# Performance work log

Measured on AMD Instinct MI355X. Metric: run time of the kernel, lower is better.

## Reference

```python
import jax, jax.numpy as jnp
import numpy as np

B, S, H = 32, 2048, 1024

def setup_inputs() -> dict:
    key = jax.random.key(0)
    ks = jax.random.split(key, 8)
    scale = 1.0 / np.sqrt(H)
    return {
        "decoder_hidden": jax.random.normal(ks[0], (B, 1, H), dtype=jnp.float32),
        "encoder_outputs": jax.random.normal(ks[1], (B, S, H), dtype=jnp.float32),
        "coverage": jax.random.uniform(ks[2], (B, S), dtype=jnp.float32),
        "W_enc": jax.random.normal(ks[3], (H, H), dtype=jnp.float32) * scale,  # enc_v.weight [out,in]
        "W_dec": jax.random.normal(ks[4], (H, H), dtype=jnp.float32) * scale,  # dec_v.weight
        "b_dec": jax.random.normal(ks[5], (H,), dtype=jnp.float32) * scale,    # dec_v.bias
        "w_cov": jax.random.normal(ks[6], (H,), dtype=jnp.float32) * scale,    # cov_v.weight [H,1] squeezed
        "v": jax.random.normal(ks[7], (H,), dtype=jnp.float32) * scale,        # V_prime.weight [1,H] squeezed
    }

def reference(decoder_hidden, encoder_outputs, coverage, W_enc, W_dec, b_dec, w_cov, v):
    # enc_feature: [B,S,H]; torch Linear is x @ W.T
    enc_feature = jnp.einsum("bsh,oh->bso", encoder_outputs, W_enc)
    # dec_feature: [B,1,H], broadcasts over S
    dec_feature = jnp.einsum("bqh,oh->bqo", decoder_hidden, W_dec) + b_dec
    # cov_feature: coverage[...,None] @ w_cov[None,:] -> [B,S,H]
    cov_feature = coverage[..., None] * w_cov
    scores = jnp.tanh(enc_feature + dec_feature + cov_feature)  # [B,S,H]
    attn_scores = jnp.einsum("bsh,h->bs", scores, v)            # V_prime, squeeze(-1)
    attn_dist = jax.nn.softmax(attn_scores, axis=-1)[:, None, :]  # [B,1,S]
    return attn_dist
```

## Files before the change

kernel.cpp:

```cpp
#include <hip/hip_runtime.h>

#define Bb 32
#define Ss 2048
#define Hh 1024

typedef __attribute__((ext_vector_type(4))) float f32x4;
typedef __attribute__((ext_vector_type(8))) short s16x8;

#define GAS const __attribute__((address_space(1))) unsigned int
#define LAS __attribute__((address_space(3))) unsigned int

__device__ __forceinline__ unsigned short f2bf(float x) {
  unsigned int u = __float_as_uint(x);
  u = (u + 0x7fffu + ((u >> 16) & 1u)) >> 16;
  return (unsigned short)u;
}

__global__ void cvt_swz_kernel(const float* __restrict__ in, unsigned short* __restrict__ out) {
  int g = blockIdx.x * blockDim.x + threadIdx.x;
  int row = g >> 7;
  int kc8 = (g & 127) << 3;
  const float4* src = reinterpret_cast<const float4*>(in + (size_t)row * Hh + kc8);
  float4 a = src[0], b = src[1];
  union { unsigned short u[8]; uint4 q; } rr;
  rr.u[0] = f2bf(a.x); rr.u[1] = f2bf(a.y); rr.u[2] = f2bf(a.z); rr.u[3] = f2bf(a.w);
  rr.u[4] = f2bf(b.x); rr.u[5] = f2bf(b.y); rr.u[6] = f2bf(b.z); rr.u[7] = f2bf(b.w);
  int r = row & 255;
  size_t byte = ((size_t)(row >> 8) * 32 + (kc8 >> 5)) * 16384
              + (size_t)(r * 64 + (((kc8 & 31) * 2) ^ ((r & 3) << 4)));
  *reinterpret_cast<uint4*>(reinterpret_cast<char*>(out) + byte) = rr.q;
}

__global__ void dec_feat_kernel(const float* __restrict__ dh,
                                const float* __restrict__ Wd,
                                const float* __restrict__ bd,
                                float* __restrict__ out) {
  int gw = blockIdx.x * 4 + (threadIdx.x >> 6);
  int lane = threadIdx.x & 63;
  int b = gw >> 10;
  int o = gw & 1023;
  const float4* x = reinterpret_cast<const float4*>(dh + (size_t)b * Hh);
  const float4* w = reinterpret_cast<const float4*>(Wd + (size_t)o * Hh);
  float acc = 0.f;
#pragma unroll
  for (int it = 0; it < 4; ++it) {
    float4 xa = x[lane + it * 64];
    float4 wa = w[lane + it * 64];
    acc += xa.x * wa.x + xa.y * wa.y + xa.z * wa.z + xa.w * wa.w;
  }
#pragma unroll
  for (int m = 1; m < 64; m <<= 1) acc += __shfl_xor(acc, m, 64);
  if (lane == 0) out[gw] = acc + bd[o];
}

__global__ void __launch_bounds__(512, 2)
gemm8(const unsigned short* __restrict__ Aw,
      const unsigned short* __restrict__ Bw,
      const float* __restrict__ decf,
      const float* __restrict__ cov,
      const float* __restrict__ wcov,
      const float* __restrict__ v,
      float* __restrict__ scores) {
  __shared__ char lds[131072];

  const int bid = blockIdx.x;
  const int swz = (bid & 7) * 128 + (bid >> 3);
  const int s_tile = swz >> 2;
  const int ot = swz & 3;

  const int tid = threadIdx.x, lane = tid & 63;
  const int wid = tid >> 6, wm = wid >> 2, wn = wid & 3;
  const int fr = lane & 15, hi = lane >> 4;

  const char* gA = reinterpret_cast<const char*>(Aw) + (size_t)s_tile * 32 * 16384 + tid * 16;
  const char* gB = reinterpret_cast<const char*>(Bw) + (size_t)ot * 32 * 16384 + tid * 16;

#define STAGE_A(t) do {                                                           \
    const char* _s = gA + (size_t)(t) * 16384;                                    \
    char* _d = lds + ((t) & 3) * 32768 + tid * 16;                                \
    __builtin_amdgcn_global_load_lds((GAS*)(_s),        (LAS*)(_d),        16, 0, 0); \
    __builtin_amdgcn_global_load_lds((GAS*)(_s + 8192), (LAS*)(_d + 8192), 16, 0, 0); \
  } while (0)
#define STAGE_B(t) do {                                                           \
    const char* _s = gB + (size_t)(t) * 16384;                                    \
    char* _d = lds + ((t) & 3) * 32768 + 16384 + tid * 16;                        \
    __builtin_amdgcn_global_load_lds((GAS*)(_s),        (LAS*)(_d),        16, 0, 0); \
    __builtin_amdgcn_global_load_lds((GAS*)(_s + 8192), (LAS*)(_d + 8192), 16, 0, 0); \
  } while (0)
#define NOSTAGE ((void)0)
#define VM4 asm volatile("s_waitcnt vmcnt(4)" ::: "memory")
#define VM0 asm volatile("s_waitcnt vmcnt(0)" ::: "memory")
#define NOWAIT ((void)0)

  const int xr = (fr & 3) << 4;
  const int aOff = wm * 8192 + fr * 64 + ((hi * 16) ^ xr);
  const int bOff = 16384 + wn * 4096 + fr * 64 + ((hi * 16) ^ xr);

  f32x4 acc[8][4];
#pragma unroll
  for (int i = 0; i < 8; ++i)
#pragma unroll
    for (int j = 0; j < 4; ++j) acc[i][j] = (f32x4){0.f, 0.f, 0.f, 0.f};

  s16x8 afrag[4], bfrag[4];

#define PH_A(t, STAGE) do {                                                       \
    const char* Lb = lds + ((t) & 3) * 32768;                                     \
    _Pragma("unroll") for (int fn = 0; fn < 4; ++fn)                              \
      bfrag[fn] = *reinterpret_cast<const s16x8*>(Lb + bOff + fn * 1024);         \
    _Pragma("unroll") for (int fm = 0; fm < 4; ++fm)                              \
      afrag[fm] = *reinterpret_cast<const s16x8*>(Lb + aOff + fm * 1024);         \
    STAGE;                                                                        \
    __builtin_amdgcn_s_barrier();                                                 \
    asm volatile("s_waitcnt lgkmcnt(0)" ::: "memory");                            \
    __builtin_amdgcn_sched_barrier(0);                                            \
    __builtin_amdgcn_s_setprio(1);                                                \
    _Pragma("unroll") for (int fm = 0; fm < 4; ++fm)                              \
      _Pragma("unroll") for (int fn = 0; fn < 4; ++fn)                            \
        acc[fm][fn] = __builtin_amdgcn_mfma_f32_16x16x32_bf16(                    \
            afrag[fm], bfrag[fn], acc[fm][fn], 0, 0, 0);                          \
    __builtin_amdgcn_s_setprio(0);                                                \
    __builtin_amdgcn_s_barrier();                                                 \
  } while (0)

#define PH_B(t, STAGE, WAIT) do {                                                 \
    const char* Lb = lds + ((t) & 3) * 32768;                                     \
    _Pragma("unroll") for (int fm = 0; fm < 4; ++fm)                              \
      afrag[fm] = *reinterpret_cast<const s16x8*>(Lb + aOff + (fm + 4) * 1024);   \
    STAGE;                                                                        \
    WAIT;                                                                         \
    __builtin_amdgcn_s_barrier();                                                 \
    asm volatile("s_waitcnt lgkmcnt(0)" ::: "memory");                            \
    __builtin_amdgcn_sched_barrier(0);                                            \
    __builtin_amdgcn_s_setprio(1);                                                \
    _Pragma("unroll") for (int fm = 0; fm < 4; ++fm)                              \
      _Pragma("unroll") for (int fn = 0; fn < 4; ++fn)                            \
        acc[fm + 4][fn] = __builtin_amdgcn_mfma_f32_16x16x32_bf16(                \
            afrag[fm], bfrag[fn], acc[fm + 4][fn], 0, 0, 0);                      \
    __builtin_amdgcn_s_setprio(0);                                                \
    __builtin_amdgcn_s_barrier();                                                 \
  } while (0)

  STAGE_A(0); STAGE_B(0);
  STAGE_A(1); STAGE_B(1);
  VM4;
  __builtin_amdgcn_s_barrier();

  for (int t = 0; t < 30; ++t) {
    PH_A(t, STAGE_A(t + 2));
    PH_B(t, STAGE_B(t + 2), VM4);
  }
  PH_A(30, NOSTAGE);
  PH_B(30, NOSTAGE, VM0);
  PH_A(31, NOSTAGE);
  PH_B(31, NOSTAGE, NOWAIT);

#undef PH_A
#undef PH_B
#undef STAGE_A
#undef STAGE_B

  const int row0 = s_tile * 256 + wm * 128 + hi * 4;
  const int o0 = ot * 256 + wn * 64 + fr;
  const int bb = s_tile >> 3;

  float vv[4], wv[4], dv[4];
#pragma unroll
  for (int fn = 0; fn < 4; ++fn) {
    int o = o0 + fn * 16;
    vv[fn] = v[o];
    wv[fn] = wcov[o];
    dv[fn] = decf[bb * 1024 + o];
  }

#pragma unroll
  for (int fm = 0; fm < 8; ++fm) {
#pragma unroll
    for (int r = 0; r < 4; ++r) {
      int s_flat = row0 + fm * 16 + r;
      float c = cov[s_flat];
      float sum = 0.f;
#pragma unroll
      for (int fn = 0; fn < 4; ++fn) {
        float x = acc[fm][fn][r] + dv[fn] + c * wv[fn];
        sum += tanhf(x) * vv[fn];
      }
      sum += __shfl_xor(sum, 1, 64);
      sum += __shfl_xor(sum, 2, 64);
      sum += __shfl_xor(sum, 4, 64);
      sum += __shfl_xor(sum, 8, 64);
      if (fr == 0) atomicAdd(&scores[s_flat], sum);
    }
  }
}

__global__ void softmax_kernel(const float* __restrict__ scores, float* __restrict__ out) {
  int b = blockIdx.x;
  int tid = threadIdx.x;
  int lane = tid & 63, w = tid >> 6;
  const float* row = scores + (size_t)b * Ss;
  float vals[8];
#pragma unroll
  for (int k = 0; k < 8; ++k) vals[k] = row[tid + k * 256];
  float m = vals[0];
#pragma unroll
  for (int k = 1; k < 8; ++k) m = fmaxf(m, vals[k]);
#pragma unroll
  for (int off = 1; off < 64; off <<= 1) m = fmaxf(m, __shfl_xor(m, off, 64));
  __shared__ float sm[4], ss[4];
  if (lane == 0) sm[w] = m;
  __syncthreads();
  m = fmaxf(fmaxf(sm[0], sm[1]), fmaxf(sm[2], sm[3]));
  float s = 0.f;
#pragma unroll
  for (int k = 0; k < 8; ++k) { vals[k] = __expf(vals[k] - m); s += vals[k]; }
#pragma unroll
  for (int off = 1; off < 64; off <<= 1) s += __shfl_xor(s, off, 64);
  if (lane == 0) ss[w] = s;
  __syncthreads();
  s = ss[0] + ss[1] + ss[2] + ss[3];
  float inv = 1.f / s;
#pragma unroll
  for (int k = 0; k < 8; ++k) out[(size_t)b * Ss + tid + k * 256] = vals[k] * inv;
}

extern "C" void kernel_launch(void* const* d_in, const int* in_sizes, int n_in,
                              void* d_out, int out_size, void* d_ws, size_t ws_size,
                              hipStream_t stream) {
  const float* dh    = (const float*)d_in[0];
  const float* enc   = (const float*)d_in[1];
  const float* cov   = (const float*)d_in[2];
  const float* W_enc = (const float*)d_in[3];
  const float* W_dec = (const float*)d_in[4];
  const float* b_dec = (const float*)d_in[5];
  const float* w_cov = (const float*)d_in[6];
  const float* v     = (const float*)d_in[7];
  float* out = (float*)d_out;

  char* ws = (char*)d_ws;
  unsigned short* A_bf  = (unsigned short*)ws;
  unsigned short* W_bf  = (unsigned short*)(ws + 134217728);
  float*          decf  = (float*)(ws + 136314880);
  float*          score = (float*)(ws + 136445952);

  hipMemsetAsync(score, 0, (size_t)Bb * Ss * sizeof(float), stream);
  cvt_swz_kernel<<<32768, 256, 0, stream>>>(enc, A_bf);
  cvt_swz_kernel<<<512, 256, 0, stream>>>(W_enc, W_bf);
  dec_feat_kernel<<<(Bb * Hh) / 4, 256, 0, stream>>>(dh, W_dec, b_dec, decf);
  gemm8<<<1024, 512, 0, stream>>>(A_bf, W_bf, decf, cov, w_cov, v, score);
  softmax_kernel<<<Bb, 256, 0, stream>>>(score, out);
}
```

Baseline: 304.4 us.

## Restructure GEMM pipeline to 64-wide K tiles with double buffering and fast tanh

The bf16 layout now packs K in 64-wide tiles split into two 32-wide halves, with a new XOR swizzle on bits of the row index. The GEMM main loop changes from quad-buffered 32-wide K steps to double-buffered 64-wide tiles. Each tile runs four phases and keeps up to seven async load groups in flight under a vmcnt(6) wait. The epilogue replaces tanhf with a clamped exp-based tanh to cut transcendental cost, at a small accuracy cost.

```diff
diff --git a/kernel.cpp b/kernel.cpp
--- a/kernel.cpp
+++ b/kernel.cpp
@@ -16,18 +16,18 @@
   return (unsigned short)u;
 }
 
-__global__ void cvt_swz_kernel(const float* __restrict__ in, unsigned short* __restrict__ out) {
+__global__ void cvt_swz(const float* __restrict__ in, unsigned short* __restrict__ out) {
   int g = blockIdx.x * blockDim.x + threadIdx.x;
-  int row = g >> 7;
-  int kc8 = (g & 127) << 3;
-  const float4* src = reinterpret_cast<const float4*>(in + (size_t)row * Hh + kc8);
+  int row = g >> 7, k8 = g & 127;
+  const float4* src = reinterpret_cast<const float4*>(in + (size_t)row * Hh + k8 * 8);
   float4 a = src[0], b = src[1];
   union { unsigned short u[8]; uint4 q; } rr;
   rr.u[0] = f2bf(a.x); rr.u[1] = f2bf(a.y); rr.u[2] = f2bf(a.z); rr.u[3] = f2bf(a.w);
   rr.u[4] = f2bf(b.x); rr.u[5] = f2bf(b.y); rr.u[6] = f2bf(b.z); rr.u[7] = f2bf(b.w);
+  int kt = k8 >> 3, kh = (k8 >> 2) & 1, k4 = k8 & 3;
   int r = row & 255;
-  size_t byte = ((size_t)(row >> 8) * 32 + (kc8 >> 5)) * 16384
-              + (size_t)(r * 64 + (((kc8 & 31) * 2) ^ ((r & 3) << 4)));
+  size_t byte = (size_t)(((row >> 8) * 16 + kt) * 2 + kh) * 16384
+              + (size_t)(r * 64 + ((k4 ^ ((r >> 1) & 3)) << 4));
   *reinterpret_cast<uint4*>(reinterpret_cast<char*>(out) + byte) = rr.q;
 }
 
@@ -37,8 +37,7 @@
                                 float* __restrict__ out) {
   int gw = blockIdx.x * 4 + (threadIdx.x >> 6);
   int lane = threadIdx.x & 63;
-  int b = gw >> 10;
-  int o = gw & 1023;
+  int b = gw >> 10, o = gw & 1023;
   const float4* x = reinterpret_cast<const float4*>(dh + (size_t)b * Hh);
   const float4* w = reinterpret_cast<const float4*>(Wd + (size_t)o * Hh);
   float acc = 0.f;
@@ -54,13 +53,13 @@
 }
 
 __global__ void __launch_bounds__(512, 2)
-gemm8(const unsigned short* __restrict__ Aw,
-      const unsigned short* __restrict__ Bw,
-      const float* __restrict__ decf,
-      const float* __restrict__ cov,
-      const float* __restrict__ wcov,
-      const float* __restrict__ v,
-      float* __restrict__ scores) {
+gemm8p(const unsigned short* __restrict__ Aw,
+       const unsigned short* __restrict__ Bw,
+       const float* __restrict__ decf,
+       const float* __restrict__ cov,
+       const float* __restrict__ wcov,
+       const float* __restrict__ v,
+       float* __restrict__ scores) {
   __shared__ char lds[131072];
 
   const int bid = blockIdx.x;
@@ -68,97 +67,75 @@
   const int s_tile = swz >> 2;
   const int ot = swz & 3;
 
-  const int tid = threadIdx.x, lane = tid & 63;
-  const int wid = tid >> 6, wm = wid >> 2, wn = wid & 3;
+  const int tid = threadIdx.x, lane = tid & 63, wid = tid >> 6;
+  const int wm = wid >> 2, wn = wid & 3;
   const int fr = lane & 15, hi = lane >> 4;
 
-  const char* gA = reinterpret_cast<const char*>(Aw) + (size_t)s_tile * 32 * 16384 + tid * 16;
-  const char* gB = reinterpret_cast<const char*>(Bw) + (size_t)ot * 32 * 16384 + tid * 16;
-
-#define STAGE_A(t) do {                                                           \
-    const char* _s = gA + (size_t)(t) * 16384;                                    \
-    char* _d = lds + ((t) & 3) * 32768 + tid * 16;                                \
-    __builtin_amdgcn_global_load_lds((GAS*)(_s),        (LAS*)(_d),        16, 0, 0); \
-    __builtin_amdgcn_global_load_lds((GAS*)(_s + 8192), (LAS*)(_d + 8192), 16, 0, 0); \
+  const char* gA = reinterpret_cast<const char*>(Aw) + (size_t)s_tile * 524288 + tid * 16;
+  const char* gB = reinterpret_cast<const char*>(Bw) + (size_t)ot * 524288 + tid * 16;
+
+  const int xslot = (hi ^ ((fr >> 1) & 3)) << 4;
+  const int aRow = (wm * 128 + fr) * 64;
+  const int bRow = 32768 + (wn * 64 + fr) * 64;
+
+#define STAGE(jj) do {                                                            \
+    int _j = (jj);                                                                \
+    if (_j < 64) {                                                                \
+      int _kt = _j >> 2, _h = _j & 3, _isB = _h & 1, _kh = _h >> 1;               \
+      const char* _src = (_isB ? gB : gA) + (size_t)(_kt * 2 + _kh) * 16384;      \
+      char* _dst = lds + (_kt & 1) * 65536 + _isB * 32768 + _kh * 16384 + tid * 16; \
+      __builtin_amdgcn_global_load_lds((GAS*)(_src),        (LAS*)(_dst),        16, 0, 0); \
+      __builtin_amdgcn_global_load_lds((GAS*)(_src + 8192), (LAS*)(_dst + 8192), 16, 0, 0); \
+    }                                                                             \
   } while (0)
-#define STAGE_B(t) do {                                                           \
-    const char* _s = gB + (size_t)(t) * 16384;                                    \
-    char* _d = lds + ((t) & 3) * 32768 + 16384 + tid * 16;                        \
-    __builtin_amdgcn_global_load_lds((GAS*)(_s),        (LAS*)(_d),        16, 0, 0); \
-    __builtin_amdgcn_global_load_lds((GAS*)(_s + 8192), (LAS*)(_d + 8192), 16, 0, 0); \
-  } while (0)
-#define NOSTAGE ((void)0)
-#define VM4 asm volatile("s_waitcnt vmcnt(4)" ::: "memory")
+
+#define NW ((void)0)
+#define VM6 asm volatile("s_waitcnt vmcnt(6)" ::: "memory")
 #define VM0 asm volatile("s_waitcnt vmcnt(0)" ::: "memory")
-#define NOWAIT ((void)0)
-
-  const int xr = (fr & 3) << 4;
-  const int aOff = wm * 8192 + fr * 64 + ((hi * 16) ^ xr);
-  const int bOff = 16384 + wn * 4096 + fr * 64 + ((hi * 16) ^ xr);
-
-  f32x4 acc[8][4];
-#pragma unroll
-  for (int i = 0; i < 8; ++i)
-#pragma unroll
-    for (int j = 0; j < 4; ++j) acc[i][j] = (f32x4){0.f, 0.f, 0.f, 0.f};
-
-  s16x8 afrag[4], bfrag[4];
-
-#define PH_A(t, STAGE) do {                                                       \
-    const char* Lb = lds + ((t) & 3) * 32768;                                     \
+#define KWAIT(t) do { if ((t) < 14) VM6; else if ((t) == 14) VM0; } while (0)
+
+#define PHASE(c, mh, kh, jj, WAIT) do {                                           \
+    const char* Lb = lds + (c) * 65536 + (kh) * 16384;                            \
+    s16x8 bfr[4], afr[4];                                                         \
     _Pragma("unroll") for (int fn = 0; fn < 4; ++fn)                              \
-      bfrag[fn] = *reinterpret_cast<const s16x8*>(Lb + bOff + fn * 1024);         \
+      bfr[fn] = *reinterpret_cast<const s16x8*>(Lb + bRow + fn * 1024 + xslot);   \
     _Pragma("unroll") for (int fm = 0; fm < 4; ++fm)                              \
-      afrag[fm] = *reinterpret_cast<const s16x8*>(Lb + aOff + fm * 1024);         \
-    STAGE;                                                                        \
+      afr[fm] = *reinterpret_cast<const s16x8*>(Lb + aRow + (mh) * 4096 + fm * 1024 + xslot); \
+    STAGE(jj);                                                                    \
     __builtin_amdgcn_s_barrier();                                                 \
     asm volatile("s_waitcnt lgkmcnt(0)" ::: "memory");                            \
     __builtin_amdgcn_sched_barrier(0);                                            \
     __builtin_amdgcn_s_setprio(1);                                                \
     _Pragma("unroll") for (int fm = 0; fm < 4; ++fm)                              \
       _Pragma("unroll") for (int fn = 0; fn < 4; ++fn)                            \
-        acc[fm][fn] = __builtin_amdgcn_mfma_f32_16x16x32_bf16(                    \
-            afrag[fm], bfrag[fn], acc[fm][fn], 0, 0, 0);                          \
+        acc[(mh) * 4 + fm][fn] = __builtin_amdgcn_mfma_f32_16x16x32_bf16(         \
+            afr[fm], bfr[fn], acc[(mh) * 4 + fm][fn], 0, 0, 0);                   \
     __builtin_amdgcn_s_setprio(0);                                                \
+    WAIT;                                                                         \
     __builtin_amdgcn_s_barrier();                                                 \
   } while (0)
 
-#define PH_B(t, STAGE, WAIT) do {                                                 \
-    const char* Lb = lds + ((t) & 3) * 32768;                                     \
-    _Pragma("unroll") for (int fm = 0; fm < 4; ++fm)                              \
-      afrag[fm] = *reinterpret_cast<const s16x8*>(Lb + aOff + (fm + 4) * 1024);   \
-    STAGE;                                                                        \
-    WAIT;                                                                         \
-    __builtin_amdgcn_s_barrier();                                                 \
-    asm volatile("s_waitcnt lgkmcnt(0)" ::: "memory");                            \
-    __builtin_amdgcn_sched_barrier(0);                                            \
-    __builtin_amdgcn_s_setprio(1);                                                \
-    _Pragma("unroll") for (int fm = 0; fm < 4; ++fm)                              \
-      _Pragma("unroll") for (int fn = 0; fn < 4; ++fn)                            \
-        acc[fm + 4][fn] = __builtin_amdgcn_mfma_f32_16x16x32_bf16(                \
-            afrag[fm], bfrag[fn], acc[fm + 4][fn], 0, 0, 0);                      \
-    __builtin_amdgcn_s_setprio(0);                                                \
-    __builtin_amdgcn_s_barrier();                                                 \
-  } while (0)
-
-  STAGE_A(0); STAGE_B(0);
-  STAGE_A(1); STAGE_B(1);
-  VM4;
+  f32x4 acc[8][4];
+#pragma unroll
+  for (int i = 0; i < 8; ++i)
+#pragma unroll
+    for (int j = 0; j < 4; ++j) acc[i][j] = (f32x4){0.f, 0.f, 0.f, 0.f};
+
+  STAGE(0); STAGE(1); STAGE(2); STAGE(3); STAGE(4); STAGE(5); STAGE(6);
+  VM6;
   __builtin_amdgcn_s_barrier();
 
-  for (int t = 0; t < 30; ++t) {
-    PH_A(t, STAGE_A(t + 2));
-    PH_B(t, STAGE_B(t + 2), VM4);
-  }
-  PH_A(30, NOSTAGE);
-  PH_B(30, NOSTAGE, VM0);
-  PH_A(31, NOSTAGE);
-  PH_B(31, NOSTAGE, NOWAIT);
-
-#undef PH_A
-#undef PH_B
-#undef STAGE_A
-#undef STAGE_B
+#pragma unroll 1
+  for (int t = 0; t < 16; ++t) {
+    const int c = t & 1;
+    const int j0 = 4 * t + 7;
+    PHASE(c, 0, 0, j0,     NW);
+    PHASE(c, 1, 0, j0 + 1, NW);
+    PHASE(c, 0, 1, j0 + 2, NW);
+    PHASE(c, 1, 1, j0 + 3, KWAIT(t));
+  }
+#undef PHASE
+#undef STAGE
 
   const int row0 = s_tile * 256 + wm * 128 + hi * 4;
   const int o0 = ot * 256 + wn * 64 + fr;
@@ -174,16 +151,18 @@
   }
 
 #pragma unroll
-  for (int fm = 0; fm < 8; ++fm) {
+  for (int i = 0; i < 8; ++i) {
 #pragma unroll
     for (int r = 0; r < 4; ++r) {
-      int s_flat = row0 + fm * 16 + r;
+      int s_flat = row0 + i * 16 + r;
       float c = cov[s_flat];
       float sum = 0.f;
 #pragma unroll
       for (int fn = 0; fn < 4; ++fn) {
-        float x = acc[fm][fn][r] + dv[fn] + c * wv[fn];
-        sum += tanhf(x) * vv[fn];
+        float x = acc[i][fn][r] + dv[fn] + c * wv[fn];
+        float xc = fminf(fmaxf(x, -15.f), 15.f);
+        float e2 = __expf(2.f * xc);
+        sum += (1.f - 2.f / (e2 + 1.f)) * vv[fn];
       }
       sum += __shfl_xor(sum, 1, 64);
       sum += __shfl_xor(sum, 2, 64);
@@ -244,9 +223,9 @@
   float*          score = (float*)(ws + 136445952);
 
   hipMemsetAsync(score, 0, (size_t)Bb * Ss * sizeof(float), stream);
-  cvt_swz_kernel<<<32768, 256, 0, stream>>>(enc, A_bf);
-  cvt_swz_kernel<<<512, 256, 0, stream>>>(W_enc, W_bf);
+  cvt_swz<<<32768, 256, 0, stream>>>(enc, A_bf);
+  cvt_swz<<<512, 256, 0, stream>>>(W_enc, W_bf);
   dec_feat_kernel<<<(Bb * Hh) / 4, 256, 0, stream>>>(dh, W_dec, b_dec, decf);
-  gemm8<<<1024, 512, 0, stream>>>(A_bf, W_bf, decf, cov, w_cov, v, score);
+  gemm8p<<<1024, 512, 0, stream>>>(A_bf, W_bf, decf, cov, w_cov, v, score);
   softmax_kernel<<<Bb, 256, 0, stream>>>(score, out);
 }
```

Result: faster. 284.2 us (-6.6%).
